# Performance work log

Measured on AMD Instinct MI355X. Metric: run time of the kernel, lower is better.

Reference implementation:

```python
import jax, jax.numpy as jnp
import numpy as np

N_GRAPHS = 500
NODES_PER_GRAPH = 100
EDGES_PER_GRAPH = 800
IN_DIM = 64
HIDDEN = 128
RATIO = 0.8
N = N_GRAPHS * NODES_PER_GRAPH          # 50000 nodes
E = N_GRAPHS * EDGES_PER_GRAPH          # 400000 edges
K = int(RATIO * EDGES_PER_GRAPH)        # 640 causal edges kept per graph


def _lin(key, fan_in, fan_out):
    return jax.random.normal(key, (fan_in, fan_out), jnp.float32) / float(np.sqrt(fan_in))


def setup_inputs() -> dict:
    key = jax.random.key(0)
    ks = jax.random.split(key, 20)
    x = jax.random.normal(ks[0], (N, IN_DIM), jnp.float32)
    src = jax.random.randint(ks[1], (N_GRAPHS, EDGES_PER_GRAPH), 0, NODES_PER_GRAPH)
    dst = jax.random.randint(ks[2], (N_GRAPHS, EDGES_PER_GRAPH), 0, NODES_PER_GRAPH)
    offs = (jnp.arange(N_GRAPHS) * NODES_PER_GRAPH)[:, None]
    edge_index = jnp.stack([(src + offs).reshape(-1), (dst + offs).reshape(-1)]).astype(jnp.int32)
    edge_attr = jax.random.normal(ks[3], (E,), jnp.float32)
    batch_idx = jnp.repeat(jnp.arange(N_GRAPHS, dtype=jnp.int32), NODES_PER_GRAPH)
    inp = dict(x=x, edge_index=edge_index, edge_attr=edge_attr, batch_idx=batch_idx)
    # LEConv1 (in_dim -> hidden): lin1 (bias), lin2 (no bias), lin3 (bias)
    inp['c1_w1'] = _lin(ks[4], IN_DIM, HIDDEN); inp['c1_b1'] = jnp.zeros((HIDDEN,), jnp.float32)
    inp['c1_w2'] = _lin(ks[5], IN_DIM, HIDDEN)
    inp['c1_w3'] = _lin(ks[6], IN_DIM, HIDDEN); inp['c1_b3'] = jnp.zeros((HIDDEN,), jnp.float32)
    # LEConv2 (hidden -> hidden)
    inp['c2_w1'] = _lin(ks[7], HIDDEN, HIDDEN); inp['c2_b1'] = jnp.zeros((HIDDEN,), jnp.float32)
    inp['c2_w2'] = _lin(ks[8], HIDDEN, HIDDEN)
    inp['c2_w3'] = _lin(ks[9], HIDDEN, HIDDEN); inp['c2_b3'] = jnp.zeros((HIDDEN,), jnp.float32)
    # edge-score MLP: Linear(2h,4h) -> ReLU -> Linear(4h,1)
    inp['mlp_w1'] = _lin(ks[10], 2 * HIDDEN, 4 * HIDDEN); inp['mlp_b1'] = jnp.zeros((4 * HIDDEN,), jnp.float32)
    inp['mlp_w2'] = _lin(ks[11], 4 * HIDDEN, 1); inp['mlp_b2'] = jnp.zeros((1,), jnp.float32)
    return inp


def leconv(x, edge_index, ew, w1, b1, w2, w3, b3):
    # PyG LEConv: out_i = sum_{j->i} w_ji * (lin1(x_j) - lin2(x_i)) + lin3(x_i)
    a = x @ w1 + b1
    b = x @ w2
    src, dst = edge_index[0], edge_index[1]
    msg = (a[src] - b[dst]) * ew[:, None]
    agg = jax.ops.segment_sum(msg, dst, num_segments=x.shape[0])
    return agg + x @ w3 + b3


def relabel(x, edge_index, batch):
    # fixed-size unique: pads with sentinel n; x/batch padded with a dummy row
    n = x.shape[0]
    sub = jnp.unique(edge_index.reshape(-1), size=n, fill_value=n)
    x_pad = jnp.concatenate([x, jnp.zeros((1, x.shape[1]), x.dtype)], axis=0)
    b_pad = jnp.concatenate([batch, jnp.full((1,), -1, batch.dtype)])
    node_idx = jnp.full((n + 1,), -1, jnp.int32).at[sub].set(jnp.arange(n, dtype=jnp.int32))
    return x_pad[sub], node_idx[edge_index], b_pad[sub]


def _forward(x, edge_index, edge_attr, batch_idx,
             c1_w1, c1_b1, c1_w2, c1_w3, c1_b3,
             c2_w1, c2_b1, c2_w2, c2_w3, c2_b3,
             mlp_w1, mlp_b1, mlp_w2, mlp_b2):
    ew = edge_attr.reshape(-1)
    h = jax.nn.relu(leconv(x, edge_index, ew, c1_w1, c1_b1, c1_w2, c1_w3, c1_b3))
    h = leconv(h, edge_index, ew, c2_w1, c2_b1, c2_w2, c2_w3, c2_b3)
    src, dst = edge_index[0], edge_index[1]
    edge_rep = jnp.concatenate([h[src], h[dst]], axis=-1)                  # [E, 2h]
    edge_score = (jax.nn.relu(edge_rep @ mlp_w1 + mlp_b1) @ mlp_w2 + mlp_b2).reshape(-1)
    # per-graph top-k split (equal-size graphs -> static [B, E_g] view)
    scores = edge_score.reshape(N_GRAPHS, EDGES_PER_GRAPH)
    order = jnp.argsort(-scores, axis=1)
    offs = (jnp.arange(N_GRAPHS) * EDGES_PER_GRAPH)[:, None]
    idx_res = (order[:, :K] + offs).reshape(-1)
    idx_drop = (order[:, K:] + offs).reshape(-1)
    c_ei = edge_index[:, idx_res]
    f_ei = edge_index[:, idx_drop]
    c_w = edge_score[idx_res]
    f_w = -edge_score[idx_drop]
    c_attr = edge_attr[idx_res]
    f_attr = edge_attr[idx_drop]
    c_x, c_ei2, c_b = relabel(h, c_ei, batch_idx)
    f_x, f_ei2, f_b = relabel(h, f_ei, batch_idx)
    return (c_x, c_ei2, c_attr, c_w, c_b, f_x, f_ei2, f_attr, f_w, f_b, edge_score)


def reference(x, edge_index, edge_attr, batch_idx,
              c1_w1, c1_b1, c1_w2, c1_w3, c1_b3,
              c2_w1, c2_b1, c2_w2, c2_w3, c2_b3,
              mlp_w1, mlp_b1, mlp_w2, mlp_b2):
    return _forward(x, edge_index, edge_attr, batch_idx,
                    c1_w1, c1_b1, c1_w2, c1_w3, c1_b3,
                    c2_w1, c2_b1, c2_w2, c2_w3, c2_b3,
                    mlp_w1, mlp_b1, mlp_w2, mlp_b2)
```

## Files before the change

### kernel.cpp

```cpp
#include <hip/hip_runtime.h>

#define NG 500
#define NPG 100
#define EPG 800
#define INDIM 64
#define HID 128
#define ETOT (NG*EPG)
#define NTOT (NG*NPG)
#define KKEEP 640
#define KDROP 160
#define MAXDEG 64

#define OFF_CX    0u
#define OFF_CEI   6400000u
#define OFF_CATTR 7040000u
#define OFF_CW    7360000u
#define OFF_CB    7680000u
#define OFF_FX    7730000u
#define OFF_FEI   14130000u
#define OFF_FATTR 14290000u
#define OFF_FW    14370000u
#define OFF_FB    14450000u
#define OFF_ES    14500000u

__global__ __launch_bounds__(128) void prep_kernel(
    const int* __restrict__ ei, const float* __restrict__ ea,
    float2* __restrict__ elist2, int* __restrict__ ecnt, float* __restrict__ sdeg)
{
  __shared__ unsigned char esrcL[EPG];
  __shared__ unsigned char edstL[EPG];
  __shared__ float ewvL[EPG];
  const int g = blockIdx.x, t = threadIdx.x;
  const int nb = g * NPG;
  for (int e = t; e < EPG; e += 128) {
    int ge = g * EPG + e;
    esrcL[e] = (unsigned char)(ei[ge] - nb);
    edstL[e] = (unsigned char)(ei[ETOT + ge] - nb);
    ewvL[e] = ea[ge];
  }
  __syncthreads();
  if (t < NPG) {
    int cnt = 0; float s = 0.f;
    float2* lp = elist2 + (size_t)(nb + t) * MAXDEG;
    for (int e = 0; e < EPG; e++) {
      if ((int)edstL[e] == t) {
        if (cnt < MAXDEG) lp[cnt] = make_float2(ewvL[e], __int_as_float((int)esrcL[e]));
        cnt++; s += ewvL[e];
      }
    }
    ecnt[nb + t] = cnt < MAXDEG ? cnt : MAXDEG;
    sdeg[nb + t] = s;
  }
}

template<int K>
__global__ __launch_bounds__(512) void preagg_kernel(
    const float* __restrict__ xin, const float2* __restrict__ elist2,
    const int* __restrict__ ecnt, float* __restrict__ y)
{
  __shared__ float xt[NPG][K];
  const int g = blockIdx.x, t = threadIdx.x;
  const int nb = g * NPG;
  for (int i = t; i < NPG * K / 4; i += 512)
    ((float4*)xt)[i] = ((const float4*)(xin + (size_t)nb * K))[i];
  __syncthreads();
  const int c = t % K, grp = t / K;
  const int NGRP = 512 / K;
  for (int d = grp; d < NPG; d += NGRP) {
    const int cn = ecnt[nb + d];
    const float2* lp = elist2 + (size_t)(nb + d) * MAXDEG;
    float acc = 0.f;
    for (int j = 0; j < cn; j++) {
      float2 p = lp[j];
      acc += p.x * xt[__float_as_int(p.y)][c];
    }
    y[(size_t)(nb + d) * K + c] = acc;
  }
}

template<int K, bool RELU>
__global__ __launch_bounds__(256) void conv_gemm_kernel(
    const float* __restrict__ y, const float* __restrict__ xin, const float* __restrict__ sdeg,
    const float* __restrict__ w1, const float* __restrict__ w2, const float* __restrict__ w3,
    const float* __restrict__ b1, const float* __restrict__ b3,
    float* __restrict__ hout)
{
  __shared__ float wl[64][HID];
  const int t = threadIdx.x;
  const int m0 = blockIdx.x * 128;
  const int tc = t % 16;
  const int tr = t / 16;
  float acc[8][8];
#pragma unroll
  for (int i = 0; i < 8; i++)
#pragma unroll
    for (int j = 0; j < 8; j++) acc[i][j] = 0.f;

  int rowc[8]; float sdv[8];
#pragma unroll
  for (int i = 0; i < 8; i++) {
    int r = m0 + tr * 8 + i;
    rowc[i] = r < NTOT ? r : NTOT - 1;
    sdv[i] = sdeg[rowc[i]];
  }
  const int NCH = (3 * K) / 64;
  for (int ch = 0; ch < NCH; ++ch) {
    __syncthreads();
    for (int i = t; i < 64 * HID / 4; i += 256) {
      int kk = i / 32, q = i % 32;
      int kr = ch * 64 + kk;
      int seg = kr / K; int sr = kr % K;
      const float* wp = seg == 0 ? w1 : (seg == 1 ? w3 : w2);
      float4 v = *(const float4*)(wp + (size_t)sr * HID + q * 4);
      if (seg == 2) { v.x = -v.x; v.y = -v.y; v.z = -v.z; v.w = -v.w; }
      *(float4*)&wl[kk][q * 4] = v;
    }
    __syncthreads();
    const int seg = (ch * 64) / K;
    const int kb = (ch * 64) % K;
    for (int k4 = 0; k4 < 16; ++k4) {
      float4 a4[8];
#pragma unroll
      for (int i = 0; i < 8; i++) {
        const float* src = (seg == 0 ? y : xin) + (size_t)rowc[i] * K + kb + k4 * 4;
        float4 v = *(const float4*)src;
        if (seg == 2) { float s = sdv[i]; v.x *= s; v.y *= s; v.z *= s; v.w *= s; }
        a4[i] = v;
      }
#pragma unroll
      for (int kk = 0; kk < 4; kk++) {
        float wv0[4], wv1[4];
        *(float4*)wv0 = *(const float4*)&wl[k4 * 4 + kk][tc * 4];
        *(float4*)wv1 = *(const float4*)&wl[k4 * 4 + kk][64 + tc * 4];
#pragma unroll
        for (int i = 0; i < 8; i++) {
          const float av = (&a4[i].x)[kk];
#pragma unroll
          for (int j = 0; j < 4; j++) {
            acc[i][j]     += av * wv0[j];
            acc[i][4 + j] += av * wv1[j];
          }
        }
      }
    }
  }
#pragma unroll
  for (int i = 0; i < 8; i++) {
    const int r = m0 + tr * 8 + i;
    if (r < NTOT) {
      float4 o0, o1;
#pragma unroll
      for (int j = 0; j < 4; j++) {
        float c0 = acc[i][j]     + sdv[i] * b1[tc * 4 + j]      + b3[tc * 4 + j];
        float c1 = acc[i][4 + j] + sdv[i] * b1[64 + tc * 4 + j] + b3[64 + tc * 4 + j];
        if (RELU) { c0 = fmaxf(c0, 0.f); c1 = fmaxf(c1, 0.f); }
        (&o0.x)[j] = c0; (&o1.x)[j] = c1;
      }
      float* op = hout + (size_t)r * HID;
      *(float4*)(op + tc * 4) = o0;
      *(float4*)(op + 64 + tc * 4) = o1;
    }
  }
}

__global__ __launch_bounds__(1024) void score_kernel(
    const float* __restrict__ h2, const int* __restrict__ ei,
    const float* __restrict__ mw1, const float* __restrict__ mb1,
    const float* __restrict__ mw2, const float* __restrict__ mb2,
    float* __restrict__ scores_ws, float* __restrict__ out_es)
{
  __shared__ float Pl[200][64];
  __shared__ float Ql[200][64];
  __shared__ float wl[HID][64];
  __shared__ float w2l[64];
  __shared__ unsigned char esrcL[2 * EPG];
  __shared__ unsigned char edstL[2 * EPG];

  const int b = blockIdx.x, t = threadIdx.x;
  const int g0 = 2 * b;
  const int rowbase = b * 200;

  for (int e = t; e < 2 * EPG; e += 1024) {
    int gi = e / EPG, el = e - gi * EPG;
    int ge = (g0 + gi) * EPG + el;
    esrcL[e] = (unsigned char)(ei[ge] - (g0 + gi) * NPG);
    edstL[e] = (unsigned char)(ei[ETOT + ge] - (g0 + gi) * NPG);
  }

  const int tc = t % 32;
  const int tr = t / 32;
  int sl0 = 0, dl0 = 0, sl1 = 0, dl1 = 0;
  double acc0 = 0., acc1 = 0.;
  const int pr = (t >> 1) & 31;

  for (int ch = 0; ch < 8; ++ch) {
    __syncthreads();
    if (ch == 0 && t < EPG) {
      sl0 = esrcL[t];        dl0 = edstL[t];
      sl1 = 100 + esrcL[EPG + t]; dl1 = 100 + edstL[EPG + t];
    }
    for (int i = t; i < HID * 16; i += 1024) {
      int k = i / 16, q = i % 16;
      *(float4*)&wl[k][q * 4] = *(const float4*)(mw1 + (size_t)k * 512 + ch * 64 + q * 4);
    }
    __syncthreads();
    if (tr < 25) {
      float a0[8], a1[8];
      const float bp0 = mb1[ch * 64 + tc * 2], bp1 = mb1[ch * 64 + tc * 2 + 1];
#pragma unroll
      for (int i = 0; i < 8; i++) { a0[i] = bp0; a1[i] = bp1; }
      for (int k4 = 0; k4 < 32; ++k4) {
        float4 a4[8];
#pragma unroll
        for (int i = 0; i < 8; i++)
          a4[i] = *(const float4*)(h2 + (size_t)(rowbase + tr * 8 + i) * HID + k4 * 4);
#pragma unroll
        for (int kk = 0; kk < 4; kk++) {
          const float2 wv = *(const float2*)&wl[k4 * 4 + kk][tc * 2];
#pragma unroll
          for (int i = 0; i < 8; i++) {
            const float av = (&a4[i].x)[kk];
            a0[i] += av * wv.x; a1[i] += av * wv.y;
          }
        }
      }
#pragma unroll
      for (int i = 0; i < 8; i++)
        *(float2*)&Pl[tr * 8 + i][tc * 2] = make_float2(a0[i], a1[i]);
    }
    __syncthreads();
    for (int i = t; i < HID * 16; i += 1024) {
      int k = i / 16, q = i % 16;
      *(float4*)&wl[k][q * 4] = *(const float4*)(mw1 + (size_t)(HID + k) * 512 + ch * 64 + q * 4);
    }
    if (t < 16) *(float4*)&w2l[t * 4] = *(const float4*)(mw2 + ch * 64 + t * 4);
    __syncthreads();
    if (tr < 25) {
      float a0[8], a1[8];
#pragma unroll
      for (int i = 0; i < 8; i++) { a0[i] = 0.f; a1[i] = 0.f; }
      for (int k4 = 0; k4 < 32; ++k4) {
        float4 a4[8];
#pragma unroll
        for (int i = 0; i < 8; i++)
          a4[i] = *(const float4*)(h2 + (size_t)(rowbase + tr * 8 + i) * HID + k4 * 4);
#pragma unroll
        for (int kk = 0; kk < 4; kk++) {
          const float2 wv = *(const float2*)&wl[k4 * 4 + kk][tc * 2];
#pragma unroll
          for (int i = 0; i < 8; i++) {
            const float av = (&a4[i].x)[kk];
            a0[i] += av * wv.x; a1[i] += av * wv.y;
          }
        }
      }
#pragma unroll
      for (int i = 0; i < 8; i++)
        *(float2*)&Ql[tr * 8 + i][tc * 2] = make_float2(a0[i], a1[i]);
    }
    __syncthreads();
    if (t < EPG) {
#pragma unroll 4
      for (int i = 0; i < 32; ++i) {
        const int j = (((pr + i) & 31) * 2);
        const float2 p0 = *(const float2*)&Pl[sl0][j];
        const float2 q0 = *(const float2*)&Ql[dl0][j];
        const float2 p1 = *(const float2*)&Pl[sl1][j];
        const float2 q1 = *(const float2*)&Ql[dl1][j];
        const float2 wv = *(const float2*)&w2l[j];
        const float s0 = fmaxf(p0.x + q0.x, 0.f) * wv.x + fmaxf(p0.y + q0.y, 0.f) * wv.y;
        const float s1 = fmaxf(p1.x + q1.x, 0.f) * wv.x + fmaxf(p1.y + q1.y, 0.f) * wv.y;
        acc0 += (double)s0; acc1 += (double)s1;
      }
    }
  }
  if (t < EPG) {
    const double b2v = (double)mb2[0];
    const float s0 = (float)(acc0 + b2v);
    const float s1 = (float)(acc1 + b2v);
    const int ge0 = g0 * EPG + t, ge1 = (g0 + 1) * EPG + t;
    scores_ws[ge0] = s0; out_es[ge0] = s0;
    scores_ws[ge1] = s1; out_es[ge1] = s1;
  }
}

__global__ __launch_bounds__(256, 1) void sort_kernel(
    const float* __restrict__ scores, const int* __restrict__ ei,
    int* __restrict__ keptEid, int* __restrict__ dropEid,
    int* __restrict__ cLocal, int* __restrict__ fLocal,
    int* __restrict__ cCount, int* __restrict__ fCount)
{
  __shared__ unsigned long long keys[1024];
  __shared__ int cpres[NPG];
  __shared__ int fpres[NPG];
  const int g = blockIdx.x, t = threadIdx.x;
  const int nb = g * NPG;

  for (int i = t; i < 1024; i += 256) {
    unsigned long long kk;
    if (i < EPG) {
      const float sc = scores[g * EPG + i];
      const unsigned int bb = __float_as_uint(sc);
      const unsigned int m = (bb & 0x80000000u) ? (~bb) : (bb | 0x80000000u);
      const unsigned int k1 = ~m;
      kk = ((unsigned long long)k1 << 32) | (unsigned int)i;
    } else {
      kk = 0xFFFFFFFFFFFFFFFFull;
    }
    keys[i] = kk;
  }
  for (int i = t; i < NPG; i += 256) { cpres[i] = 0; fpres[i] = 0; }
  __syncthreads();

  for (int k = 2; k <= 1024; k <<= 1) {
    for (int j = k >> 1; j > 0; j >>= 1) {
      for (int i = t; i < 1024; i += 256) {
        const int l = i ^ j;
        if (l > i) {
          const bool up = ((i & k) == 0);
          const unsigned long long va = keys[i], vb = keys[l];
          if ((va > vb) == up) { keys[i] = vb; keys[l] = va; }
        }
      }
      __syncthreads();
    }
  }

  for (int r = t; r < EPG; r += 256) {
    const int el = (int)(unsigned int)keys[r];
    const int ge = g * EPG + el;
    const int sl = ei[ge] - nb, dl = ei[ETOT + ge] - nb;
    if (r < KKEEP) {
      keptEid[g * KKEEP + r] = ge;
      cpres[sl] = 1; cpres[dl] = 1;
    } else {
      dropEid[g * KDROP + (r - KKEEP)] = ge;
      fpres[sl] = 1; fpres[dl] = 1;
    }
  }
  __syncthreads();

  if (t == 0) {
    int cc = 0;
    for (int v = 0; v < NPG; v++) { const int p = cpres[v]; cLocal[nb + v] = p ? cc : -1; cc += p; }
    cCount[g] = cc;
  }
  if (t == 64) {
    int fc = 0;
    for (int v = 0; v < NPG; v++) { const int p = fpres[v]; fLocal[nb + v] = p ? fc : -1; fc += p; }
    fCount[g] = fc;
  }
}

__global__ __launch_bounds__(512) void offsets_kernel(
    const int* __restrict__ cCount, const int* __restrict__ fCount,
    int* __restrict__ cOff, int* __restrict__ fOff)
{
  __shared__ int sc[512];
  __shared__ int sf[512];
  const int t = threadIdx.x;
  const int c0 = (t < NG) ? cCount[t] : 0;
  const int f0 = (t < NG) ? fCount[t] : 0;
  sc[t] = c0; sf[t] = f0;
  __syncthreads();
  for (int off = 1; off < 512; off <<= 1) {
    const int ac = (t >= off) ? sc[t - off] : 0;
    const int af = (t >= off) ? sf[t - off] : 0;
    __syncthreads();
    sc[t] += ac; sf[t] += af;
    __syncthreads();
  }
  if (t < NG) { cOff[t] = sc[t] - c0; fOff[t] = sf[t] - f0; }
  if (t == NG - 1) { cOff[NG] = sc[t]; fOff[NG] = sf[t]; }
}

__global__ __launch_bounds__(256) void scatter_kernel(
    const float* __restrict__ h2, const int* __restrict__ cLocal, const int* __restrict__ fLocal,
    const int* __restrict__ cOff, const int* __restrict__ fOff,
    int* __restrict__ nodeIdxC, int* __restrict__ nodeIdxF, float* __restrict__ out)
{
  const int tid = blockIdx.x * 256 + threadIdx.x;
  if (tid >= 2 * NTOT * 32) return;
  const int side = tid >= NTOT * 32 ? 1 : 0;
  const int rem = tid - side * NTOT * 32;
  const int v = rem >> 5, q = rem & 31;
  const int loc = side ? fLocal[v] : cLocal[v];
  if (loc < 0) return;
  const int g = v / NPG;
  const int pos = (side ? fOff[g] : cOff[g]) + loc;
  const float4* srcv = (const float4*)(h2 + (size_t)v * HID);
  float4* dstv = (float4*)(out + (side ? OFF_FX : OFF_CX) + (size_t)pos * HID);
  dstv[q] = srcv[q];
  if (q == 0) {
    (side ? nodeIdxF : nodeIdxC)[v] = pos;
    out[(side ? OFF_FB : OFF_CB) + pos] = (float)g;
  }
}

__global__ __launch_bounds__(256) void fill_kernel(
    const int* __restrict__ cOff, const int* __restrict__ fOff, float* __restrict__ out)
{
  const int tid = blockIdx.x * 256 + threadIdx.x;
  if (tid >= 2 * NTOT * 32) return;
  const int side = tid >= NTOT * 32 ? 1 : 0;
  const int rem = tid - side * NTOT * 32;
  const int r = rem >> 5, q = rem & 31;
  const int total = side ? fOff[NG] : cOff[NG];
  if (r < total) return;
  float4 z; z.x = 0.f; z.y = 0.f; z.z = 0.f; z.w = 0.f;
  ((float4*)(out + (side ? OFF_FX : OFF_CX)))[(size_t)r * 32 + q] = z;
  if (q == 0) out[(side ? OFF_FB : OFF_CB) + r] = -1.0f;
}

__global__ __launch_bounds__(256) void edgeout_kernel(
    const int* __restrict__ ei, const float* __restrict__ ea, const float* __restrict__ scores,
    const int* __restrict__ keptEid, const int* __restrict__ dropEid,
    const int* __restrict__ nodeIdxC, const int* __restrict__ nodeIdxF, float* __restrict__ out)
{
  const int tid = blockIdx.x * 256 + threadIdx.x;
  if (tid >= ETOT) return;
  if (tid < NG * KKEEP) {
    const int ge = keptEid[tid];
    out[OFF_CEI + tid] = (float)nodeIdxC[ei[ge]];
    out[OFF_CEI + 320000 + tid] = (float)nodeIdxC[ei[ETOT + ge]];
    out[OFF_CATTR + tid] = ea[ge];
    out[OFF_CW + tid] = scores[ge];
  } else {
    const int i = tid - NG * KKEEP;
    const int ge = dropEid[i];
    out[OFF_FEI + i] = (float)nodeIdxF[ei[ge]];
    out[OFF_FEI + 80000 + i] = (float)nodeIdxF[ei[ETOT + ge]];
    out[OFF_FATTR + i] = ea[ge];
    out[OFF_FW + i] = -scores[ge];
  }
}

extern "C" void kernel_launch(void* const* d_in, const int* in_sizes, int n_in,
                              void* d_out, int out_size, void* d_ws, size_t ws_size,
                              hipStream_t stream) {
  const float* x    = (const float*)d_in[0];
  const int*   ei   = (const int*)d_in[1];
  const float* ea   = (const float*)d_in[2];
  const float* c1w1 = (const float*)d_in[4];
  const float* c1b1 = (const float*)d_in[5];
  const float* c1w2 = (const float*)d_in[6];
  const float* c1w3 = (const float*)d_in[7];
  const float* c1b3 = (const float*)d_in[8];
  const float* c2w1 = (const float*)d_in[9];
  const float* c2b1 = (const float*)d_in[10];
  const float* c2w2 = (const float*)d_in[11];
  const float* c2w3 = (const float*)d_in[12];
  const float* c2b3 = (const float*)d_in[13];
  const float* mw1  = (const float*)d_in[14];
  const float* mb1  = (const float*)d_in[15];
  const float* mw2  = (const float*)d_in[16];
  const float* mb2  = (const float*)d_in[17];
  float* out = (float*)d_out;

  char* p = (char*)d_ws;
  auto carve = [&](size_t bytes) { void* r = (void*)p; p += (bytes + 255) & ~(size_t)255; return r; };
  float* h1      = (float*)carve((size_t)NTOT * HID * 4);
  float* h2      = (float*)carve((size_t)NTOT * HID * 4);
  float* ybuf    = (float*)carve((size_t)NTOT * HID * 4);
  float* scores  = (float*)carve((size_t)ETOT * 4);
  int* keptEid   = (int*)carve((size_t)NG * KKEEP * 4);
  int* dropEid   = (int*)carve((size_t)NG * KDROP * 4);
  int* cLocal    = (int*)carve((size_t)NTOT * 4);
  int* fLocal    = (int*)carve((size_t)NTOT * 4);
  int* cCount    = (int*)carve((size_t)NG * 4);
  int* fCount    = (int*)carve((size_t)NG * 4);
  int* cOff      = (int*)carve((size_t)(NG + 1) * 4);
  int* fOff      = (int*)carve((size_t)(NG + 1) * 4);
  int* nodeIdxC  = (int*)carve((size_t)NTOT * 4);
  int* nodeIdxF  = (int*)carve((size_t)NTOT * 4);
  float2* elist2 = (float2*)carve((size_t)NTOT * MAXDEG * 8);
  int* ecnt      = (int*)carve((size_t)NTOT * 4);
  float* sdeg    = (float*)carve((size_t)NTOT * 4);

  const int MT = (NTOT + 127) / 128;

  prep_kernel<<<NG, 128, 0, stream>>>(ei, ea, elist2, ecnt, sdeg);
  preagg_kernel<INDIM><<<NG, 512, 0, stream>>>(x, elist2, ecnt, ybuf);
  conv_gemm_kernel<INDIM, true><<<MT, 256, 0, stream>>>(ybuf, x, sdeg, c1w1, c1w2, c1w3, c1b1, c1b3, h1);
  preagg_kernel<HID><<<NG, 512, 0, stream>>>(h1, elist2, ecnt, ybuf);
  conv_gemm_kernel<HID, false><<<MT, 256, 0, stream>>>(ybuf, h1, sdeg, c2w1, c2w2, c2w3, c2b1, c2b3, h2);
  score_kernel<<<NG / 2, 1024, 0, stream>>>(h2, ei, mw1, mb1, mw2, mb2, scores, out + OFF_ES);
  sort_kernel<<<NG, 256, 0, stream>>>(scores, ei, keptEid, dropEid, cLocal, fLocal, cCount, fCount);
  offsets_kernel<<<1, 512, 0, stream>>>(cCount, fCount, cOff, fOff);
  const int sc_threads = 2 * NTOT * 32;
  scatter_kernel<<<(sc_threads + 255) / 256, 256, 0, stream>>>(h2, cLocal, fLocal, cOff, fOff, nodeIdxC, nodeIdxF, out);
  fill_kernel<<<(sc_threads + 255) / 256, 256, 0, stream>>>(cOff, fOff, out);
  edgeout_kernel<<<(ETOT + 255) / 256, 256, 0, stream>>>(ei, ea, scores, keptEid, dropEid, nodeIdxC, nodeIdxF, out);
}
```

Measured before the change: 913.2 us.

## Split edge-score MLP into full-grid node GEMM and fused edge-score+sort kernel

Replaces the per-graph-pair score kernel, which used 250 blocks of 1024 threads and recomputed P/Q projections in 8 chunks, with a separate tiled GEMM over all nodes. That GEMM writes a 50000x1024 P|Q buffer. The edge scoring (ReLU dot with mw2) is then fused into the sort kernel, which reads P/Q per graph from global memory and sorts without a separate scores pass. The aim is more parallelism for the GEMM and one fewer launch with its round trip. The cost is roughly 200MB of extra global writes and reads for the PQ buffer, which is aliased over the earlier h1/ybuf workspace.

```diff
diff --git a/kernel.cpp b/kernel.cpp
--- a/kernel.cpp
+++ b/kernel.cpp
@@ -163,153 +163,153 @@
   }
 }
 
-__global__ __launch_bounds__(1024) void score_kernel(
-    const float* __restrict__ h2, const int* __restrict__ ei,
-    const float* __restrict__ mw1, const float* __restrict__ mb1,
-    const float* __restrict__ mw2, const float* __restrict__ mb2,
-    float* __restrict__ scores_ws, float* __restrict__ out_es)
-{
-  __shared__ float Pl[200][64];
-  __shared__ float Ql[200][64];
-  __shared__ float wl[HID][64];
-  __shared__ float w2l[64];
-  __shared__ unsigned char esrcL[2 * EPG];
-  __shared__ unsigned char edstL[2 * EPG];
-
-  const int b = blockIdx.x, t = threadIdx.x;
-  const int g0 = 2 * b;
-  const int rowbase = b * 200;
-
-  for (int e = t; e < 2 * EPG; e += 1024) {
-    int gi = e / EPG, el = e - gi * EPG;
-    int ge = (g0 + gi) * EPG + el;
-    esrcL[e] = (unsigned char)(ei[ge] - (g0 + gi) * NPG);
-    edstL[e] = (unsigned char)(ei[ETOT + ge] - (g0 + gi) * NPG);
-  }
-
-  const int tc = t % 32;
-  const int tr = t / 32;
-  int sl0 = 0, dl0 = 0, sl1 = 0, dl1 = 0;
-  double acc0 = 0., acc1 = 0.;
-  const int pr = (t >> 1) & 31;
-
-  for (int ch = 0; ch < 8; ++ch) {
-    __syncthreads();
-    if (ch == 0 && t < EPG) {
-      sl0 = esrcL[t];        dl0 = edstL[t];
-      sl1 = 100 + esrcL[EPG + t]; dl1 = 100 + edstL[EPG + t];
-    }
-    for (int i = t; i < HID * 16; i += 1024) {
-      int k = i / 16, q = i % 16;
-      *(float4*)&wl[k][q * 4] = *(const float4*)(mw1 + (size_t)k * 512 + ch * 64 + q * 4);
-    }
-    __syncthreads();
-    if (tr < 25) {
-      float a0[8], a1[8];
-      const float bp0 = mb1[ch * 64 + tc * 2], bp1 = mb1[ch * 64 + tc * 2 + 1];
-#pragma unroll
-      for (int i = 0; i < 8; i++) { a0[i] = bp0; a1[i] = bp1; }
-      for (int k4 = 0; k4 < 32; ++k4) {
-        float4 a4[8];
-#pragma unroll
-        for (int i = 0; i < 8; i++)
-          a4[i] = *(const float4*)(h2 + (size_t)(rowbase + tr * 8 + i) * HID + k4 * 4);
-#pragma unroll
-        for (int kk = 0; kk < 4; kk++) {
-          const float2 wv = *(const float2*)&wl[k4 * 4 + kk][tc * 2];
-#pragma unroll
-          for (int i = 0; i < 8; i++) {
-            const float av = (&a4[i].x)[kk];
-            a0[i] += av * wv.x; a1[i] += av * wv.y;
+__global__ __launch_bounds__(256) void pq_gemm_kernel(
+    const float* __restrict__ h2, const float* __restrict__ mw1, const float* __restrict__ mb1,
+    float* __restrict__ PQ)
+{
+  __shared__ float wl[64][HID];
+  const int t = threadIdx.x;
+  const int m0 = blockIdx.x * 128;
+  const int n0 = blockIdx.y * 128;
+  const int tc = t % 16, tr = t / 16;
+  const int basek = (n0 >= 512) ? HID : 0;
+  const int cbase = n0 & 511;
+
+  float acc[8][8];
+#pragma unroll
+  for (int i = 0; i < 8; i++) {
+#pragma unroll
+    for (int j = 0; j < 4; j++) {
+      acc[i][j]     = (basek == 0) ? mb1[n0 + tc * 4 + j] : 0.f;
+      acc[i][4 + j] = (basek == 0) ? mb1[n0 + 64 + tc * 4 + j] : 0.f;
+    }
+  }
+  int rowc[8];
+#pragma unroll
+  for (int i = 0; i < 8; i++) {
+    int r = m0 + tr * 8 + i;
+    rowc[i] = r < NTOT ? r : NTOT - 1;
+  }
+
+  for (int ch = 0; ch < 2; ++ch) {
+    __syncthreads();
+    for (int i = t; i < 64 * 32; i += 256) {
+      int kk = i / 32, q = i % 32;
+      *(float4*)&wl[kk][q * 4] =
+          *(const float4*)(mw1 + (size_t)(basek + ch * 64 + kk) * 512 + cbase + q * 4);
+    }
+    __syncthreads();
+    for (int k4 = 0; k4 < 16; ++k4) {
+      float4 a4[8];
+#pragma unroll
+      for (int i = 0; i < 8; i++)
+        a4[i] = *(const float4*)(h2 + (size_t)rowc[i] * HID + ch * 64 + k4 * 4);
+#pragma unroll
+      for (int kk = 0; kk < 4; kk++) {
+        float wv0[4], wv1[4];
+        *(float4*)wv0 = *(const float4*)&wl[k4 * 4 + kk][tc * 4];
+        *(float4*)wv1 = *(const float4*)&wl[k4 * 4 + kk][64 + tc * 4];
+#pragma unroll
+        for (int i = 0; i < 8; i++) {
+          const float av = (&a4[i].x)[kk];
+#pragma unroll
+          for (int j = 0; j < 4; j++) {
+            acc[i][j]     += av * wv0[j];
+            acc[i][4 + j] += av * wv1[j];
           }
         }
       }
-#pragma unroll
-      for (int i = 0; i < 8; i++)
-        *(float2*)&Pl[tr * 8 + i][tc * 2] = make_float2(a0[i], a1[i]);
-    }
-    __syncthreads();
-    for (int i = t; i < HID * 16; i += 1024) {
-      int k = i / 16, q = i % 16;
-      *(float4*)&wl[k][q * 4] = *(const float4*)(mw1 + (size_t)(HID + k) * 512 + ch * 64 + q * 4);
-    }
-    if (t < 16) *(float4*)&w2l[t * 4] = *(const float4*)(mw2 + ch * 64 + t * 4);
-    __syncthreads();
-    if (tr < 25) {
-      float a0[8], a1[8];
-#pragma unroll
-      for (int i = 0; i < 8; i++) { a0[i] = 0.f; a1[i] = 0.f; }
-      for (int k4 = 0; k4 < 32; ++k4) {
-        float4 a4[8];
-#pragma unroll
-        for (int i = 0; i < 8; i++)
-          a4[i] = *(const float4*)(h2 + (size_t)(rowbase + tr * 8 + i) * HID + k4 * 4);
-#pragma unroll
-        for (int kk = 0; kk < 4; kk++) {
-          const float2 wv = *(const float2*)&wl[k4 * 4 + kk][tc * 2];
-#pragma unroll
-          for (int i = 0; i < 8; i++) {
-            const float av = (&a4[i].x)[kk];
-            a0[i] += av * wv.x; a1[i] += av * wv.y;
-          }
-        }
-      }
-#pragma unroll
-      for (int i = 0; i < 8; i++)
-        *(float2*)&Ql[tr * 8 + i][tc * 2] = make_float2(a0[i], a1[i]);
-    }
-    __syncthreads();
-    if (t < EPG) {
-#pragma unroll 4
-      for (int i = 0; i < 32; ++i) {
-        const int j = (((pr + i) & 31) * 2);
-        const float2 p0 = *(const float2*)&Pl[sl0][j];
-        const float2 q0 = *(const float2*)&Ql[dl0][j];
-        const float2 p1 = *(const float2*)&Pl[sl1][j];
-        const float2 q1 = *(const float2*)&Ql[dl1][j];
-        const float2 wv = *(const float2*)&w2l[j];
-        const float s0 = fmaxf(p0.x + q0.x, 0.f) * wv.x + fmaxf(p0.y + q0.y, 0.f) * wv.y;
-        const float s1 = fmaxf(p1.x + q1.x, 0.f) * wv.x + fmaxf(p1.y + q1.y, 0.f) * wv.y;
-        acc0 += (double)s0; acc1 += (double)s1;
-      }
-    }
-  }
-  if (t < EPG) {
-    const double b2v = (double)mb2[0];
-    const float s0 = (float)(acc0 + b2v);
-    const float s1 = (float)(acc1 + b2v);
-    const int ge0 = g0 * EPG + t, ge1 = (g0 + 1) * EPG + t;
-    scores_ws[ge0] = s0; out_es[ge0] = s0;
-    scores_ws[ge1] = s1; out_es[ge1] = s1;
-  }
-}
-
-__global__ __launch_bounds__(256, 1) void sort_kernel(
-    const float* __restrict__ scores, const int* __restrict__ ei,
+    }
+  }
+#pragma unroll
+  for (int i = 0; i < 8; i++) {
+    const int r = m0 + tr * 8 + i;
+    if (r < NTOT) {
+      float* op = PQ + (size_t)r * 1024 + n0;
+      *(float4*)(op + tc * 4)      = *(float4*)&acc[i][0];
+      *(float4*)(op + 64 + tc * 4) = *(float4*)&acc[i][4];
+    }
+  }
+}
+
+__global__ __launch_bounds__(256) void edge_sort_kernel(
+    const float* __restrict__ PQ, const int* __restrict__ ei,
+    const float* __restrict__ mw2, const float* __restrict__ mb2,
+    float* __restrict__ scores_ws, float* __restrict__ out_es,
     int* __restrict__ keptEid, int* __restrict__ dropEid,
     int* __restrict__ cLocal, int* __restrict__ fLocal,
     int* __restrict__ cCount, int* __restrict__ fCount)
 {
+  __shared__ float Pl[NPG][68];
+  __shared__ float Ql[NPG][68];
+  __shared__ float w2l[64];
+  __shared__ unsigned char esrcL[EPG];
+  __shared__ unsigned char edstL[EPG];
   __shared__ unsigned long long keys[1024];
   __shared__ int cpres[NPG];
   __shared__ int fpres[NPG];
+
   const int g = blockIdx.x, t = threadIdx.x;
   const int nb = g * NPG;
 
-  for (int i = t; i < 1024; i += 256) {
-    unsigned long long kk;
-    if (i < EPG) {
-      const float sc = scores[g * EPG + i];
+  for (int e = t; e < EPG; e += 256) {
+    int ge = g * EPG + e;
+    esrcL[e] = (unsigned char)(ei[ge] - nb);
+    edstL[e] = (unsigned char)(ei[ETOT + ge] - nb);
+  }
+  for (int i = t; i < NPG; i += 256) { cpres[i] = 0; fpres[i] = 0; }
+  __syncthreads();
+
+  int sl[4], dl[4];
+#pragma unroll
+  for (int m = 0; m < 4; m++) {
+    const int e = t + 256 * m;
+    const int ec = e < EPG ? e : 0;
+    sl[m] = esrcL[ec]; dl[m] = edstL[ec];
+  }
+  double accd[4];
+#pragma unroll
+  for (int m = 0; m < 4; m++) accd[m] = 0.;
+
+  for (int ch = 0; ch < 8; ++ch) {
+    __syncthreads();
+    for (int i = t; i < NPG * 16; i += 256) {
+      const int r = i >> 4, q = i & 15;
+      const float* src = PQ + (size_t)(nb + r) * 1024 + ch * 64 + q * 4;
+      *(float4*)&Pl[r][q * 4] = *(const float4*)src;
+      *(float4*)&Ql[r][q * 4] = *(const float4*)(src + 512);
+    }
+    if (t < 16) *(float4*)&w2l[t * 4] = *(const float4*)(mw2 + ch * 64 + t * 4);
+    __syncthreads();
+#pragma unroll
+    for (int m = 0; m < 4; m++) {
+      double aa = 0.;
+      for (int j4 = 0; j4 < 16; ++j4) {
+        const float4 p = *(const float4*)&Pl[sl[m]][j4 * 4];
+        const float4 q = *(const float4*)&Ql[dl[m]][j4 * 4];
+        const float4 w = *(const float4*)&w2l[j4 * 4];
+        const float s = fmaxf(p.x + q.x, 0.f) * w.x + fmaxf(p.y + q.y, 0.f) * w.y
+                      + fmaxf(p.z + q.z, 0.f) * w.z + fmaxf(p.w + q.w, 0.f) * w.w;
+        aa += (double)s;
+      }
+      accd[m] += aa;
+    }
+  }
+
+  const double b2v = (double)mb2[0];
+#pragma unroll
+  for (int m = 0; m < 4; m++) {
+    const int e = t + 256 * m;
+    if (e < EPG) {
+      const float sc = (float)(accd[m] + b2v);
+      const int ge = g * EPG + e;
+      scores_ws[ge] = sc; out_es[ge] = sc;
       const unsigned int bb = __float_as_uint(sc);
-      const unsigned int m = (bb & 0x80000000u) ? (~bb) : (bb | 0x80000000u);
-      const unsigned int k1 = ~m;
-      kk = ((unsigned long long)k1 << 32) | (unsigned int)i;
-    } else {
-      kk = 0xFFFFFFFFFFFFFFFFull;
-    }
-    keys[i] = kk;
-  }
-  for (int i = t; i < NPG; i += 256) { cpres[i] = 0; fpres[i] = 0; }
+      const unsigned int mm = (bb & 0x80000000u) ? (~bb) : (bb | 0x80000000u);
+      keys[e] = ((unsigned long long)(~mm) << 32) | (unsigned int)e;
+    }
+  }
+  if (t >= 32) keys[t + 768] = 0xFFFFFFFFFFFFFFFFull;
   __syncthreads();
 
   for (int k = 2; k <= 1024; k <<= 1) {
@@ -329,25 +329,25 @@
   for (int r = t; r < EPG; r += 256) {
     const int el = (int)(unsigned int)keys[r];
     const int ge = g * EPG + el;
-    const int sl = ei[ge] - nb, dl = ei[ETOT + ge] - nb;
+    const int s0 = esrcL[el], d0 = edstL[el];
     if (r < KKEEP) {
       keptEid[g * KKEEP + r] = ge;
-      cpres[sl] = 1; cpres[dl] = 1;
+      cpres[s0] = 1; cpres[d0] = 1;
     } else {
       dropEid[g * KDROP + (r - KKEEP)] = ge;
-      fpres[sl] = 1; fpres[dl] = 1;
+      fpres[s0] = 1; fpres[d0] = 1;
     }
   }
   __syncthreads();
 
   if (t == 0) {
     int cc = 0;
-    for (int v = 0; v < NPG; v++) { const int p = cpres[v]; cLocal[nb + v] = p ? cc : -1; cc += p; }
+    for (int v = 0; v < NPG; v++) { const int pr = cpres[v]; cLocal[nb + v] = pr ? cc : -1; cc += pr; }
     cCount[g] = cc;
   }
   if (t == 64) {
     int fc = 0;
-    for (int v = 0; v < NPG; v++) { const int p = fpres[v]; fLocal[nb + v] = p ? fc : -1; fc += p; }
+    for (int v = 0; v < NPG; v++) { const int pr = fpres[v]; fLocal[nb + v] = pr ? fc : -1; fc += pr; }
     fCount[g] = fc;
   }
 }
@@ -459,9 +459,7 @@
 
   char* p = (char*)d_ws;
   auto carve = [&](size_t bytes) { void* r = (void*)p; p += (bytes + 255) & ~(size_t)255; return r; };
-  float* h1      = (float*)carve((size_t)NTOT * HID * 4);
   float* h2      = (float*)carve((size_t)NTOT * HID * 4);
-  float* ybuf    = (float*)carve((size_t)NTOT * HID * 4);
   float* scores  = (float*)carve((size_t)ETOT * 4);
   int* keptEid   = (int*)carve((size_t)NG * KKEEP * 4);
   int* dropEid   = (int*)carve((size_t)NG * KDROP * 4);
@@ -473,9 +471,13 @@
   int* fOff      = (int*)carve((size_t)(NG + 1) * 4);
   int* nodeIdxC  = (int*)carve((size_t)NTOT * 4);
   int* nodeIdxF  = (int*)carve((size_t)NTOT * 4);
-  float2* elist2 = (float2*)carve((size_t)NTOT * MAXDEG * 8);
-  int* ecnt      = (int*)carve((size_t)NTOT * 4);
-  float* sdeg    = (float*)carve((size_t)NTOT * 4);
+  char* ub = (char*)carve((size_t)NTOT * 1024 * 4);
+  float* PQ      = (float*)ub;
+  float* h1      = (float*)ub;
+  float* ybuf    = (float*)(ub + (size_t)NTOT * HID * 4);
+  float2* elist2 = (float2*)(ub + (size_t)2 * NTOT * HID * 4);
+  int* ecnt      = (int*)(ub + (size_t)2 * NTOT * HID * 4 + (size_t)NTOT * MAXDEG * 8);
+  float* sdeg    = (float*)(ub + (size_t)2 * NTOT * HID * 4 + (size_t)NTOT * MAXDEG * 8 + (size_t)NTOT * 4);
 
   const int MT = (NTOT + 127) / 128;
 
@@ -484,8 +486,10 @@
   conv_gemm_kernel<INDIM, true><<<MT, 256, 0, stream>>>(ybuf, x, sdeg, c1w1, c1w2, c1w3, c1b1, c1b3, h1);
   preagg_kernel<HID><<<NG, 512, 0, stream>>>(h1, elist2, ecnt, ybuf);
   conv_gemm_kernel<HID, false><<<MT, 256, 0, stream>>>(ybuf, h1, sdeg, c2w1, c2w2, c2w3, c2b1, c2b3, h2);
-  score_kernel<<<NG / 2, 1024, 0, stream>>>(h2, ei, mw1, mb1, mw2, mb2, scores, out + OFF_ES);
-  sort_kernel<<<NG, 256, 0, stream>>>(scores, ei, keptEid, dropEid, cLocal, fLocal, cCount, fCount);
+  dim3 pqgrid(MT, 8);
+  pq_gemm_kernel<<<pqgrid, 256, 0, stream>>>(h2, mw1, mb1, PQ);
+  edge_sort_kernel<<<NG, 256, 0, stream>>>(PQ, ei, mw2, mb2, scores, out + OFF_ES,
+                                           keptEid, dropEid, cLocal, fLocal, cCount, fCount);
   offsets_kernel<<<1, 512, 0, stream>>>(cCount, fCount, cOff, fOff);
   const int sc_threads = 2 * NTOT * 32;
   scatter_kernel<<<(sc_threads + 255) / 256, 256, 0, stream>>>(h2, cLocal, fLocal, cOff, fOff, nodeIdxC, nodeIdxF, out);
```

Result: faster. 833.1 us (-8.8%).

## Fuse edge scoring with per-graph sort and stage GEMM A-tiles in LDS

Applied to the files above, without the earlier changes.

The separate score and sort kernels become one kernel that runs a 1024-thread block per graph. Each block caches that graph's h2 rows in LDS, computes the P and Q projections in chunks, scores the edges and then bitonic-sorts them in place. This removes a launch and the round trip of scores through global memory, and lets the sort use one thread per key. Separately, conv_gemm now stages each 128x64 A tile in padded shared memory instead of having every thread load rows from global, at the cost of more LDS and possibly lower occupancy.

```diff
diff --git a/kernel.cpp b/kernel.cpp
--- a/kernel.cpp
+++ b/kernel.cpp
@@ -86,6 +86,7 @@
     float* __restrict__ hout)
 {
   __shared__ float wl[64][HID];
+  __shared__ float al[128][68];
   const int t = threadIdx.x;
   const int m0 = blockIdx.x * 128;
   const int tc = t % 16;
@@ -106,27 +107,33 @@
   const int NCH = (3 * K) / 64;
   for (int ch = 0; ch < NCH; ++ch) {
     __syncthreads();
+    const int seg = (ch * 64) / K;
+    const int kb = (ch * 64) % K;
     for (int i = t; i < 64 * HID / 4; i += 256) {
       int kk = i / 32, q = i % 32;
       int kr = ch * 64 + kk;
-      int seg = kr / K; int sr = kr % K;
+      int sr = kr % K;
       const float* wp = seg == 0 ? w1 : (seg == 1 ? w3 : w2);
       float4 v = *(const float4*)(wp + (size_t)sr * HID + q * 4);
       if (seg == 2) { v.x = -v.x; v.y = -v.y; v.z = -v.z; v.w = -v.w; }
       *(float4*)&wl[kk][q * 4] = v;
     }
-    __syncthreads();
-    const int seg = (ch * 64) / K;
-    const int kb = (ch * 64) % K;
+    {
+      const float* abase = (seg == 0 ? y : xin);
+      for (int i = t; i < 128 * 16; i += 256) {
+        int r = i / 16, q = i % 16;
+        int gr = m0 + r; if (gr >= NTOT) gr = NTOT - 1;
+        float4 v = *(const float4*)(abase + (size_t)gr * K + kb + q * 4);
+        if (seg == 2) { float s = sdeg[gr]; v.x *= s; v.y *= s; v.z *= s; v.w *= s; }
+        *(float4*)&al[r][q * 4] = v;
+      }
+    }
+    __syncthreads();
     for (int k4 = 0; k4 < 16; ++k4) {
       float4 a4[8];
 #pragma unroll
-      for (int i = 0; i < 8; i++) {
-        const float* src = (seg == 0 ? y : xin) + (size_t)rowc[i] * K + kb + k4 * 4;
-        float4 v = *(const float4*)src;
-        if (seg == 2) { float s = sdv[i]; v.x *= s; v.y *= s; v.z *= s; v.w *= s; }
-        a4[i] = v;
-      }
+      for (int i = 0; i < 8; i++)
+        a4[i] = *(const float4*)&al[tr * 8 + i][k4 * 4];
 #pragma unroll
       for (int kk = 0; kk < 4; kk++) {
         float wv0[4], wv1[4];
@@ -163,191 +170,147 @@
   }
 }
 
-__global__ __launch_bounds__(1024) void score_kernel(
+__global__ __launch_bounds__(1024) void score_sort_kernel(
     const float* __restrict__ h2, const int* __restrict__ ei,
     const float* __restrict__ mw1, const float* __restrict__ mb1,
     const float* __restrict__ mw2, const float* __restrict__ mb2,
-    float* __restrict__ scores_ws, float* __restrict__ out_es)
-{
-  __shared__ float Pl[200][64];
-  __shared__ float Ql[200][64];
-  __shared__ float wl[HID][64];
-  __shared__ float w2l[64];
-  __shared__ unsigned char esrcL[2 * EPG];
-  __shared__ unsigned char edstL[2 * EPG];
-
-  const int b = blockIdx.x, t = threadIdx.x;
-  const int g0 = 2 * b;
-  const int rowbase = b * 200;
-
-  for (int e = t; e < 2 * EPG; e += 1024) {
-    int gi = e / EPG, el = e - gi * EPG;
-    int ge = (g0 + gi) * EPG + el;
-    esrcL[e] = (unsigned char)(ei[ge] - (g0 + gi) * NPG);
-    edstL[e] = (unsigned char)(ei[ETOT + ge] - (g0 + gi) * NPG);
-  }
-
-  const int tc = t % 32;
-  const int tr = t / 32;
-  int sl0 = 0, dl0 = 0, sl1 = 0, dl1 = 0;
-  double acc0 = 0., acc1 = 0.;
-  const int pr = (t >> 1) & 31;
-
-  for (int ch = 0; ch < 8; ++ch) {
-    __syncthreads();
-    if (ch == 0 && t < EPG) {
-      sl0 = esrcL[t];        dl0 = edstL[t];
-      sl1 = 100 + esrcL[EPG + t]; dl1 = 100 + edstL[EPG + t];
-    }
-    for (int i = t; i < HID * 16; i += 1024) {
-      int k = i / 16, q = i % 16;
-      *(float4*)&wl[k][q * 4] = *(const float4*)(mw1 + (size_t)k * 512 + ch * 64 + q * 4);
-    }
-    __syncthreads();
-    if (tr < 25) {
-      float a0[8], a1[8];
-      const float bp0 = mb1[ch * 64 + tc * 2], bp1 = mb1[ch * 64 + tc * 2 + 1];
-#pragma unroll
-      for (int i = 0; i < 8; i++) { a0[i] = bp0; a1[i] = bp1; }
-      for (int k4 = 0; k4 < 32; ++k4) {
-        float4 a4[8];
-#pragma unroll
-        for (int i = 0; i < 8; i++)
-          a4[i] = *(const float4*)(h2 + (size_t)(rowbase + tr * 8 + i) * HID + k4 * 4);
-#pragma unroll
-        for (int kk = 0; kk < 4; kk++) {
-          const float2 wv = *(const float2*)&wl[k4 * 4 + kk][tc * 2];
-#pragma unroll
-          for (int i = 0; i < 8; i++) {
-            const float av = (&a4[i].x)[kk];
-            a0[i] += av * wv.x; a1[i] += av * wv.y;
-          }
-        }
-      }
-#pragma unroll
-      for (int i = 0; i < 8; i++)
-        *(float2*)&Pl[tr * 8 + i][tc * 2] = make_float2(a0[i], a1[i]);
-    }
-    __syncthreads();
-    for (int i = t; i < HID * 16; i += 1024) {
-      int k = i / 16, q = i % 16;
-      *(float4*)&wl[k][q * 4] = *(const float4*)(mw1 + (size_t)(HID + k) * 512 + ch * 64 + q * 4);
-    }
-    if (t < 16) *(float4*)&w2l[t * 4] = *(const float4*)(mw2 + ch * 64 + t * 4);
-    __syncthreads();
-    if (tr < 25) {
-      float a0[8], a1[8];
-#pragma unroll
-      for (int i = 0; i < 8; i++) { a0[i] = 0.f; a1[i] = 0.f; }
-      for (int k4 = 0; k4 < 32; ++k4) {
-        float4 a4[8];
-#pragma unroll
-        for (int i = 0; i < 8; i++)
-          a4[i] = *(const float4*)(h2 + (size_t)(rowbase + tr * 8 + i) * HID + k4 * 4);
-#pragma unroll
-        for (int kk = 0; kk < 4; kk++) {
-          const float2 wv = *(const float2*)&wl[k4 * 4 + kk][tc * 2];
-#pragma unroll
-          for (int i = 0; i < 8; i++) {
-            const float av = (&a4[i].x)[kk];
-            a0[i] += av * wv.x; a1[i] += av * wv.y;
-          }
-        }
-      }
-#pragma unroll
-      for (int i = 0; i < 8; i++)
-        *(float2*)&Ql[tr * 8 + i][tc * 2] = make_float2(a0[i], a1[i]);
-    }
-    __syncthreads();
-    if (t < EPG) {
-#pragma unroll 4
-      for (int i = 0; i < 32; ++i) {
-        const int j = (((pr + i) & 31) * 2);
-        const float2 p0 = *(const float2*)&Pl[sl0][j];
-        const float2 q0 = *(const float2*)&Ql[dl0][j];
-        const float2 p1 = *(const float2*)&Pl[sl1][j];
-        const float2 q1 = *(const float2*)&Ql[dl1][j];
-        const float2 wv = *(const float2*)&w2l[j];
-        const float s0 = fmaxf(p0.x + q0.x, 0.f) * wv.x + fmaxf(p0.y + q0.y, 0.f) * wv.y;
-        const float s1 = fmaxf(p1.x + q1.x, 0.f) * wv.x + fmaxf(p1.y + q1.y, 0.f) * wv.y;
-        acc0 += (double)s0; acc1 += (double)s1;
-      }
-    }
-  }
-  if (t < EPG) {
-    const double b2v = (double)mb2[0];
-    const float s0 = (float)(acc0 + b2v);
-    const float s1 = (float)(acc1 + b2v);
-    const int ge0 = g0 * EPG + t, ge1 = (g0 + 1) * EPG + t;
-    scores_ws[ge0] = s0; out_es[ge0] = s0;
-    scores_ws[ge1] = s1; out_es[ge1] = s1;
-  }
-}
-
-__global__ __launch_bounds__(256, 1) void sort_kernel(
-    const float* __restrict__ scores, const int* __restrict__ ei,
+    float* __restrict__ scores_ws, float* __restrict__ out_es,
     int* __restrict__ keptEid, int* __restrict__ dropEid,
     int* __restrict__ cLocal, int* __restrict__ fLocal,
     int* __restrict__ cCount, int* __restrict__ fCount)
 {
+  __shared__ float h2t[NPG][HID];
+  __shared__ float wl[HID][66];
+  __shared__ float Pl[NPG][34];
+  __shared__ float Ql[NPG][34];
+  __shared__ float w2l[512];
+  __shared__ unsigned char esrcL[EPG];
+  __shared__ unsigned char edstL[EPG];
   __shared__ unsigned long long keys[1024];
   __shared__ int cpres[NPG];
   __shared__ int fpres[NPG];
+
   const int g = blockIdx.x, t = threadIdx.x;
   const int nb = g * NPG;
 
-  for (int i = t; i < 1024; i += 256) {
-    unsigned long long kk;
-    if (i < EPG) {
-      const float sc = scores[g * EPG + i];
-      const unsigned int bb = __float_as_uint(sc);
-      const unsigned int m = (bb & 0x80000000u) ? (~bb) : (bb | 0x80000000u);
-      const unsigned int k1 = ~m;
-      kk = ((unsigned long long)k1 << 32) | (unsigned int)i;
-    } else {
-      kk = 0xFFFFFFFFFFFFFFFFull;
-    }
-    keys[i] = kk;
-  }
-  for (int i = t; i < NPG; i += 256) { cpres[i] = 0; fpres[i] = 0; }
+  for (int i = t; i < NPG * HID / 4; i += 1024)
+    ((float4*)h2t)[i] = ((const float4*)(h2 + (size_t)nb * HID))[i];
+  if (t < EPG) {
+    int ge = g * EPG + t;
+    esrcL[t] = (unsigned char)(ei[ge] - nb);
+    edstL[t] = (unsigned char)(ei[ETOT + ge] - nb);
+  }
+  if (t < 128) *(float4*)&w2l[t * 4] = *(const float4*)(mw2 + t * 4);
+  if (t < NPG) { cpres[t] = 0; fpres[t] = 0; }
+  __syncthreads();
+
+  const int tc = t & 31, tr = t >> 5;
+  const int isQ = tc >> 4;
+  const int cj = (tc & 15) * 2;
+  const int wcol = isQ * 32 + cj;
+  int sl = 0, dl = 0;
+  if (t < EPG) { sl = esrcL[t]; dl = edstL[t]; }
+  double accd = 0.;
+
+  for (int ch = 0; ch < 16; ++ch) {
+    for (int i = t; i < HID * 16; i += 1024) {
+      const int k = i >> 4, q = i & 15;
+      const float* src = (q < 8)
+        ? (mw1 + (size_t)k * 512 + ch * 32 + q * 4)
+        : (mw1 + (size_t)(HID + k) * 512 + ch * 32 + (q - 8) * 4);
+      *(float4*)&wl[k][q * 4] = *(const float4*)src;
+    }
+    __syncthreads();
+    if (tr < 25) {
+      float acc0[4], acc1[4];
+      const float b0 = isQ ? 0.f : mb1[ch * 32 + cj];
+      const float b1v = isQ ? 0.f : mb1[ch * 32 + cj + 1];
+#pragma unroll
+      for (int i = 0; i < 4; i++) { acc0[i] = b0; acc1[i] = b1v; }
+      for (int k4 = 0; k4 < 32; ++k4) {
+        float4 a4[4];
+#pragma unroll
+        for (int i = 0; i < 4; i++)
+          a4[i] = *(const float4*)&h2t[tr * 4 + i][k4 * 4];
+#pragma unroll
+        for (int kk = 0; kk < 4; kk++) {
+          const float2 wv = *(const float2*)&wl[k4 * 4 + kk][wcol];
+#pragma unroll
+          for (int i = 0; i < 4; i++) {
+            const float av = (&a4[i].x)[kk];
+            acc0[i] += av * wv.x; acc1[i] += av * wv.y;
+          }
+        }
+      }
+#pragma unroll
+      for (int i = 0; i < 4; i++) {
+        float* dst = isQ ? &Ql[tr * 4 + i][cj] : &Pl[tr * 4 + i][cj];
+        *(float2*)dst = make_float2(acc0[i], acc1[i]);
+      }
+    }
+    __syncthreads();
+    if (t < EPG) {
+#pragma unroll 2
+      for (int jg = 0; jg < 8; ++jg) {
+        const float2 pa = *(const float2*)&Pl[sl][jg * 4];
+        const float2 pb = *(const float2*)&Pl[sl][jg * 4 + 2];
+        const float2 qa = *(const float2*)&Ql[dl][jg * 4];
+        const float2 qb = *(const float2*)&Ql[dl][jg * 4 + 2];
+        const float* w = &w2l[ch * 32 + jg * 4];
+        const float s = fmaxf(pa.x + qa.x, 0.f) * w[0] + fmaxf(pa.y + qa.y, 0.f) * w[1]
+                      + fmaxf(pb.x + qb.x, 0.f) * w[2] + fmaxf(pb.y + qb.y, 0.f) * w[3];
+        accd += (double)s;
+      }
+    }
+    __syncthreads();
+  }
+
+  if (t < EPG) {
+    const float sc = (float)(accd + (double)mb2[0]);
+    const int ge = g * EPG + t;
+    scores_ws[ge] = sc; out_es[ge] = sc;
+    const unsigned int bb = __float_as_uint(sc);
+    const unsigned int mm = (bb & 0x80000000u) ? (~bb) : (bb | 0x80000000u);
+    keys[t] = ((unsigned long long)(~mm) << 32) | (unsigned int)t;
+  } else {
+    keys[t] = 0xFFFFFFFFFFFFFFFFull;
+  }
   __syncthreads();
 
   for (int k = 2; k <= 1024; k <<= 1) {
     for (int j = k >> 1; j > 0; j >>= 1) {
-      for (int i = t; i < 1024; i += 256) {
-        const int l = i ^ j;
-        if (l > i) {
-          const bool up = ((i & k) == 0);
-          const unsigned long long va = keys[i], vb = keys[l];
-          if ((va > vb) == up) { keys[i] = vb; keys[l] = va; }
-        }
+      const int l = t ^ j;
+      if (l > t) {
+        const bool up = ((t & k) == 0);
+        const unsigned long long va = keys[t], vb = keys[l];
+        if ((va > vb) == up) { keys[t] = vb; keys[l] = va; }
       }
       __syncthreads();
     }
   }
 
-  for (int r = t; r < EPG; r += 256) {
-    const int el = (int)(unsigned int)keys[r];
+  if (t < EPG) {
+    const int el = (int)(unsigned int)keys[t];
     const int ge = g * EPG + el;
-    const int sl = ei[ge] - nb, dl = ei[ETOT + ge] - nb;
-    if (r < KKEEP) {
-      keptEid[g * KKEEP + r] = ge;
-      cpres[sl] = 1; cpres[dl] = 1;
+    const int s0 = esrcL[el], d0 = edstL[el];
+    if (t < KKEEP) {
+      keptEid[g * KKEEP + t] = ge;
+      cpres[s0] = 1; cpres[d0] = 1;
     } else {
-      dropEid[g * KDROP + (r - KKEEP)] = ge;
-      fpres[sl] = 1; fpres[dl] = 1;
+      dropEid[g * KDROP + (t - KKEEP)] = ge;
+      fpres[s0] = 1; fpres[d0] = 1;
     }
   }
   __syncthreads();
 
   if (t == 0) {
     int cc = 0;
-    for (int v = 0; v < NPG; v++) { const int p = cpres[v]; cLocal[nb + v] = p ? cc : -1; cc += p; }
+    for (int v = 0; v < NPG; v++) { const int pr = cpres[v]; cLocal[nb + v] = pr ? cc : -1; cc += pr; }
     cCount[g] = cc;
   }
   if (t == 64) {
     int fc = 0;
-    for (int v = 0; v < NPG; v++) { const int p = fpres[v]; fLocal[nb + v] = p ? fc : -1; fc += p; }
+    for (int v = 0; v < NPG; v++) { const int pr = fpres[v]; fLocal[nb + v] = pr ? fc : -1; fc += pr; }
     fCount[g] = fc;
   }
 }
@@ -484,8 +447,8 @@
   conv_gemm_kernel<INDIM, true><<<MT, 256, 0, stream>>>(ybuf, x, sdeg, c1w1, c1w2, c1w3, c1b1, c1b3, h1);
   preagg_kernel<HID><<<NG, 512, 0, stream>>>(h1, elist2, ecnt, ybuf);
   conv_gemm_kernel<HID, false><<<MT, 256, 0, stream>>>(ybuf, h1, sdeg, c2w1, c2w2, c2w3, c2b1, c2b3, h2);
-  score_kernel<<<NG / 2, 1024, 0, stream>>>(h2, ei, mw1, mb1, mw2, mb2, scores, out + OFF_ES);
-  sort_kernel<<<NG, 256, 0, stream>>>(scores, ei, keptEid, dropEid, cLocal, fLocal, cCount, fCount);
+  score_sort_kernel<<<NG, 1024, 0, stream>>>(h2, ei, mw1, mb1, mw2, mb2, scores, out + OFF_ES,
+                                             keptEid, dropEid, cLocal, fLocal, cCount, fCount);
   offsets_kernel<<<1, 512, 0, stream>>>(cCount, fCount, cOff, fOff);
   const int sc_threads = 2 * NTOT * 32;
   scatter_kernel<<<(sc_threads + 255) / 256, 256, 0, stream>>>(h2, cLocal, fLocal, cOff, fOff, nodeIdxC, nodeIdxF, out);
```

Measured after the change: 778.9 us. 1.17x faster.
